# Optimization experiments

Hardware: AMD Instinct MI355X
Metric: run time of the kernel (lower is better)

## Reference

```python
import jax, jax.numpy as jnp
import numpy as np

Z_DIM, C_DIM = 256, 256
H = 96            # hidden_size = input_size = out_channel_num
L = 4             # num_layers
T = 239           # seq_len
B = 4096          # batch


def _gru_layer(x_seq, h0, wi, wh, bi, bh):
    """PyTorch-convention GRU layer. x_seq: [T,B,H], h0: [B,H].
    wi, wh: [3H,H] ordered (r,z,n); bi, bh: [3H]."""
    gi_seq = jnp.einsum('tbh,gh->tbg', x_seq, wi) + bi  # [T,B,3H], precomputed

    def step(h, gi):
        gh = h @ wh.T + bh
        i_r, i_z, i_n = jnp.split(gi, 3, axis=-1)
        h_r, h_z, h_n = jnp.split(gh, 3, axis=-1)
        r = jax.nn.sigmoid(i_r + h_r)
        z = jax.nn.sigmoid(i_z + h_z)
        n = jnp.tanh(i_n + r * h_n)
        h_new = (1.0 - z) * n + z * h
        return h_new, h_new

    _, out = jax.lax.scan(step, h0, gi_seq)
    return out  # [T,B,H]


def setup_inputs() -> dict:
    key = jax.random.key(0)
    ks = jax.random.split(key, 8)
    z = jax.random.normal(ks[0], (B, Z_DIM), dtype=jnp.float32)
    c = jax.random.normal(ks[1], (B, C_DIM), dtype=jnp.float32)
    s_fc = 1.0 / np.sqrt(Z_DIM + C_DIM)
    s_h = 1.0 / np.sqrt(H)
    fc1_w = jax.random.normal(ks[2], (L * H, Z_DIM + C_DIM), dtype=jnp.float32) * s_fc
    fc1_b = jax.random.normal(ks[3], (L * H,), dtype=jnp.float32) * s_fc
    w_ih = jax.random.normal(ks[4], (L, 3 * H, H), dtype=jnp.float32) * s_h
    w_hh = jax.random.normal(ks[5], (L, 3 * H, H), dtype=jnp.float32) * s_h
    b_ih = jax.random.normal(ks[6], (L, 3 * H), dtype=jnp.float32) * s_h
    b_hh = jax.random.normal(ks[7], (L, 3 * H), dtype=jnp.float32) * s_h
    return {"z": z, "c": c, "fc1_w": fc1_w, "fc1_b": fc1_b,
            "w_ih": w_ih, "w_hh": w_hh, "b_ih": b_ih, "b_hh": b_hh}


def reference(z, c, fc1_w, fc1_b, w_ih, w_hh, b_ih, b_hh):
    x = jnp.concatenate((z, c), axis=1)                 # [B, 512]
    h = x @ fc1_w.T + fc1_b                             # [B, 4H]
    h = jnp.where(h >= 0, h, 0.2 * h)                   # LeakyReLU(0.2)
    h0 = h.reshape(L, x.shape[0], H)                    # matches torch .view(L,B,H)
    seq = jnp.zeros((T, x.shape[0], H), dtype=x.dtype)  # GRU input is zeros
    for l in range(L):
        seq = _gru_layer(seq, h0[l], w_ih[l], w_hh[l], b_ih[l], b_hh[l])
    # fc2 output is computed but discarded in the original forward
    return jnp.transpose(seq, (1, 2, 0))                # [B, H, T]
```

## Files before the change

### kernel.cpp

```cpp
#include <hip/hip_runtime.h>
#include <stdint.h>

#define HDIM 96
#define G3   288
#define TLEN 239
#define BB   16
#define NBLK 256
#define NTHR 768

typedef _Float16 f16;
typedef f16  f16x8 __attribute__((ext_vector_type(8)));
typedef f16  f16x4 __attribute__((ext_vector_type(4)));
typedef float f32x4 __attribute__((ext_vector_type(4)));

__device__ __forceinline__ float sigm(float x)  { return 1.f / (1.f + __expf(-x)); }
__device__ __forceinline__ float tanh_(float x) { return 1.f - 2.f / (1.f + __expf(2.f * x)); }

template<bool HAS_X>
__global__ __launch_bounds__(NTHR, 3)
void gru_layer(float* seq,
               const float* __restrict__ zin, const float* __restrict__ cin,
               const float* __restrict__ fc1w, const float* __restrict__ fc1b,
               const float* __restrict__ wih, const float* __restrict__ whh,
               const float* __restrict__ bih, const float* __restrict__ bhh,
               int layer)
{
  __shared__ f16   h_plane[2][16][104];
  __shared__ float gi_buf[16][300];
  __shared__ float xcat[4][512];
  __shared__ float fc1o[4][384];

  const int tid = threadIdx.x;
  const int wv  = tid >> 6;
  const int ln  = tid & 63;
  const int r0  = blockIdx.x * BB;
  const int g   = ln >> 4;
  const int lm  = ln & 15;

  const int base_in = layer * 1024 + (r0 >> 2);
  for (int i = tid; i < 4 * 512; i += NTHR) {
    int q = i >> 9, k = i & 511;
    xcat[q][k] = (k < 256) ? zin[(base_in + q) * 256 + k]
                           : cin[(base_in + q) * 256 + (k - 256)];
  }
  __syncthreads();
  for (int of = wv * 32; of < wv * 32 + 32; ++of) {
    float wreg[8];
    #pragma unroll
    for (int i = 0; i < 8; ++i) wreg[i] = fc1w[of * 512 + ln + 64 * i];
    float s[4];
    #pragma unroll
    for (int q = 0; q < 4; ++q) {
      float a = 0.f;
      #pragma unroll
      for (int i = 0; i < 8; ++i) a += wreg[i] * xcat[q][ln + 64 * i];
      s[q] = a;
    }
    #pragma unroll
    for (int off = 32; off; off >>= 1)
      #pragma unroll
      for (int q = 0; q < 4; ++q) s[q] += __shfl_down(s[q], off);
    if (ln == 0) {
      float b = fc1b[of];
      #pragma unroll
      for (int q = 0; q < 4; ++q) {
        float v = s[q] + b;
        fc1o[q][of] = (v >= 0.f) ? v : 0.2f * v;
      }
    }
  }
  __syncthreads();

  const bool is_gh = (wv < 6);
  const int  wg    = is_gh ? wv : wv - 6;
  const int  col   = wg * 16 + lm;

  f16x8 wf[3][3];
  if (is_gh || HAS_X) {
    const float* wmat = is_gh ? whh : wih;
    #pragma unroll
    for (int nt = 0; nt < 3; ++nt)
      #pragma unroll
      for (int kt = 0; kt < 3; ++kt) {
        const float* src = wmat + (nt * 96 + col) * 96 + kt * 32 + 4 * g;
        f16x8 f;
        #pragma unroll
        for (int j = 0; j < 4; ++j) { f[j] = (f16)src[j]; f[4 + j] = (f16)src[16 + j]; }
        wf[nt][kt] = f;
      }
  }

  float bir = 0, biz = 0, bin_ = 0, bhr = 0, bhz = 0, bhn = 0;
  float hprev[4] = {0, 0, 0, 0};
  uint32_t obase[4] = {0, 0, 0, 0};
  if (is_gh) {
    bir = bih[col]; biz = bih[96 + col]; bin_ = bih[192 + col];
    bhr = bhh[col]; bhz = bhh[96 + col]; bhn = bhh[192 + col];
    #pragma unroll
    for (int j = 0; j < 4; ++j) {
      float h0v = fc1o[g][j * 96 + col];
      hprev[j] = h0v;
      h_plane[0][4 * g + j][col] = (f16)h0v;
      obase[j] = ((uint32_t)(r0 + 4 * g + j) * 96 + col) * 239;
    }
  }

  const float* xptr[6];
  float xc[6][4];
  if (!is_gh && HAS_X) {
    #pragma unroll
    for (int kt = 0; kt < 3; ++kt)
      #pragma unroll
      for (int hh = 0; hh < 2; ++hh) {
        int k = kt * 32 + 16 * hh + 4 * g;
        xptr[kt * 2 + hh] = seq + ((size_t)(r0 + lm) * 96 + k) * 239;
      }
    #pragma unroll
    for (int f = 0; f < 6; ++f)
      #pragma unroll
      for (int j = 0; j < 4; ++j) xc[f][j] = xptr[f][j * 239];
  }
  __syncthreads();

  float hist[4][8];
  for (int t0 = 0; t0 < TLEN; t0 += 8) {
    const int nsteps = (TLEN - t0 < 8) ? (TLEN - t0) : 8;
    #pragma unroll
    for (int s = 0; s < 8; ++s) {
      if (s < nsteps) {
        const int t = t0 + s;
        const int buf = t & 1;
        const f32x4 z4 = {0.f, 0.f, 0.f, 0.f};
        f32x4 acc[3] = {z4, z4, z4};

        if (is_gh) {
          #pragma unroll
          for (int kt = 0; kt < 3; ++kt) {
            f16x4 lo = *(const f16x4*)&h_plane[buf][lm][kt * 32 + 4 * g];
            f16x4 hi = *(const f16x4*)&h_plane[buf][lm][kt * 32 + 16 + 4 * g];
            f16x8 a;
            #pragma unroll
            for (int j = 0; j < 4; ++j) { a[j] = lo[j]; a[4 + j] = hi[j]; }
            #pragma unroll
            for (int nt = 0; nt < 3; ++nt)
              acc[nt] = __builtin_amdgcn_mfma_f32_16x16x32_f16(a, wf[nt][kt], acc[nt], 0, 0, 0);
          }
        } else if (HAS_X) {
          #pragma unroll
          for (int kt = 0; kt < 3; ++kt) {
            f16x8 a;
            #pragma unroll
            for (int j = 0; j < 4; ++j) { a[j] = (f16)xc[2 * kt][j]; a[4 + j] = (f16)xc[2 * kt + 1][j]; }
            #pragma unroll
            for (int nt = 0; nt < 3; ++nt)
              acc[nt] = __builtin_amdgcn_mfma_f32_16x16x32_f16(a, wf[nt][kt], acc[nt], 0, 0, 0);
          }
          #pragma unroll
          for (int nt = 0; nt < 3; ++nt)
            #pragma unroll
            for (int reg = 0; reg < 4; ++reg)
              gi_buf[4 * g + reg][nt * 96 + col] = acc[nt][reg];
          if (t + 1 < TLEN) {
            #pragma unroll
            for (int f = 0; f < 6; ++f)
              #pragma unroll
              for (int j = 0; j < 4; ++j) xc[f][j] = xptr[f][(t + 1) + j * 239];
          }
        }
        __syncthreads();

        if (is_gh) {
          #pragma unroll
          for (int reg = 0; reg < 4; ++reg) {
            float gr = acc[0][reg] + bhr;
            float gz = acc[1][reg] + bhz;
            float gn = acc[2][reg] + bhn;
            float ir = bir, iz = biz, in_ = bin_;
            if (HAS_X) {
              ir  += gi_buf[4 * g + reg][col];
              iz  += gi_buf[4 * g + reg][96 + col];
              in_ += gi_buf[4 * g + reg][192 + col];
            }
            float r  = sigm(ir + gr);
            float zg = sigm(iz + gz);
            float n  = tanh_(in_ + r * gn);
            float hn = (1.f - zg) * n + zg * hprev[reg];
            hprev[reg] = hn;
            hist[reg][s] = hn;
            h_plane[buf ^ 1][4 * g + reg][col] = (f16)hn;
          }
        }
        __syncthreads();
      }
    }
    if (is_gh) {
      #pragma unroll
      for (int reg = 0; reg < 4; ++reg)
        #pragma unroll
        for (int q = 0; q < 8; ++q)
          if (q < nsteps) seq[obase[reg] + (uint32_t)(t0 + q)] = hist[reg][q];
    }
  }
}

extern "C" void kernel_launch(void* const* d_in, const int* in_sizes, int n_in,
                              void* d_out, int out_size, void* d_ws, size_t ws_size,
                              hipStream_t stream) {
  const float* zin  = (const float*)d_in[0];
  const float* cin  = (const float*)d_in[1];
  const float* fc1w = (const float*)d_in[2];
  const float* fc1b = (const float*)d_in[3];
  const float* wih  = (const float*)d_in[4];
  const float* whh  = (const float*)d_in[5];
  const float* bih  = (const float*)d_in[6];
  const float* bhh  = (const float*)d_in[7];
  float* seq = (float*)d_out;
  (void)d_ws; (void)ws_size; (void)in_sizes; (void)n_in; (void)out_size;

  dim3 grid(NBLK), blk(NTHR);
  gru_layer<false><<<grid, blk, 0, stream>>>(seq, zin, cin, fc1w, fc1b,
                                             wih, whh, bih, bhh, 0);
  for (int l = 1; l < 4; ++l)
    gru_layer<true><<<grid, blk, 0, stream>>>(seq, zin, cin, fc1w, fc1b,
                                              wih + l * G3 * HDIM, whh + l * G3 * HDIM,
                                              bih + l * G3, bhh + l * G3, l);
}
```

Baseline: 12.55 ms.

## Store intermediate GRU layers as time-major fp16 in workspace, transpose final output via LDS

Intermediate layer outputs are now written as fp16 in a time-major [T,B,H] layout, in the workspace and in the unused second half of the output buffer. The next layer reads them as contiguous vector loads, double-buffered two steps ahead, instead of reading fp32 elements at a stride of 239. The final layer keeps a 32-step ring of hidden states in LDS and writes 32-step chunks to the [B,H,T] output with nontemporal stores. The aim is to cut uncoalesced global traffic and halve the bytes moved between layers. In exchange the final output is rounded through fp16, the LDS footprint grows a lot, and the old in-place path remains only as a fallback when the workspace is too small.

Result: slower. 19.94 ms (+58.8%).

```diff
diff --git a/kernel.cpp b/kernel.cpp
--- a/kernel.cpp
+++ b/kernel.cpp
@@ -7,6 +7,10 @@
 #define BB   16
 #define NBLK 256
 #define NTHR 768
+#define TSLAB (4096 * 96)
+
+#define HSLOT 1668
+#define HROW  104
 
 typedef _Float16 f16;
 typedef f16  f16x8 __attribute__((ext_vector_type(8)));
@@ -16,16 +20,16 @@
 __device__ __forceinline__ float sigm(float x)  { return 1.f / (1.f + __expf(-x)); }
 __device__ __forceinline__ float tanh_(float x) { return 1.f - 2.f / (1.f + __expf(2.f * x)); }
 
-template<bool HAS_X>
+template<bool HAS_X, bool FINAL_OUT>
 __global__ __launch_bounds__(NTHR, 3)
-void gru_layer(float* seq,
-               const float* __restrict__ zin, const float* __restrict__ cin,
-               const float* __restrict__ fc1w, const float* __restrict__ fc1b,
-               const float* __restrict__ wih, const float* __restrict__ whh,
-               const float* __restrict__ bih, const float* __restrict__ bhh,
-               int layer)
+void gru_layer_tm(const f16* __restrict__ xin, void* __restrict__ outp,
+                  const float* __restrict__ zin, const float* __restrict__ cin,
+                  const float* __restrict__ fc1w, const float* __restrict__ fc1b,
+                  const float* __restrict__ wih, const float* __restrict__ whh,
+                  const float* __restrict__ bih, const float* __restrict__ bhh,
+                  int layer)
 {
-  __shared__ f16   h_plane[2][16][104];
+  __shared__ f16   hbuf[32][HSLOT];
   __shared__ float gi_buf[16][300];
   __shared__ float xcat[4][512];
   __shared__ float fc1o[4][384];
@@ -92,6 +96,203 @@
 
   float bir = 0, biz = 0, bin_ = 0, bhr = 0, bhz = 0, bhn = 0;
   float hprev[4] = {0, 0, 0, 0};
+  if (is_gh) {
+    bir = bih[col]; biz = bih[96 + col]; bin_ = bih[192 + col];
+    bhr = bhh[col]; bhz = bhh[96 + col]; bhn = bhh[192 + col];
+    #pragma unroll
+    for (int j = 0; j < 4; ++j) {
+      float h0v = fc1o[g][j * 96 + col];
+      hprev[j] = h0v;
+      hbuf[31][(4 * g + j) * HROW + col] = (f16)h0v;
+    }
+  }
+
+  f16x4 xa[2][6];
+  size_t xoff = (size_t)(r0 + lm) * 96;
+  if (!is_gh && HAS_X) {
+    #pragma unroll
+    for (int pb = 0; pb < 2; ++pb) {
+      const f16* p = xin + (size_t)pb * TSLAB + xoff;
+      #pragma unroll
+      for (int kt = 0; kt < 3; ++kt) {
+        xa[pb][kt * 2]     = *(const f16x4*)(p + kt * 32 + 4 * g);
+        xa[pb][kt * 2 + 1] = *(const f16x4*)(p + kt * 32 + 16 + 4 * g);
+      }
+    }
+  }
+  __syncthreads();
+
+  f16*   out16 = (f16*)outp;
+  float* outf  = (float*)outp;
+
+  for (int t = 0; t < TLEN; ++t) {
+    const int slot_r = (t + 31) & 31;
+    const int slot_w = t & 31;
+    const f32x4 z4 = {0.f, 0.f, 0.f, 0.f};
+    f32x4 acc[3] = {z4, z4, z4};
+
+    if (is_gh) {
+      #pragma unroll
+      for (int kt = 0; kt < 3; ++kt) {
+        f16x4 lo = *(const f16x4*)&hbuf[slot_r][lm * HROW + kt * 32 + 4 * g];
+        f16x4 hi = *(const f16x4*)&hbuf[slot_r][lm * HROW + kt * 32 + 16 + 4 * g];
+        f16x8 a;
+        #pragma unroll
+        for (int j = 0; j < 4; ++j) { a[j] = lo[j]; a[4 + j] = hi[j]; }
+        #pragma unroll
+        for (int nt = 0; nt < 3; ++nt)
+          acc[nt] = __builtin_amdgcn_mfma_f32_16x16x32_f16(a, wf[nt][kt], acc[nt], 0, 0, 0);
+      }
+    } else if (HAS_X) {
+      const int cur = t & 1;
+      #pragma unroll
+      for (int kt = 0; kt < 3; ++kt) {
+        f16x4 lo = xa[cur][kt * 2], hi = xa[cur][kt * 2 + 1];
+        f16x8 a;
+        #pragma unroll
+        for (int j = 0; j < 4; ++j) { a[j] = lo[j]; a[4 + j] = hi[j]; }
+        #pragma unroll
+        for (int nt = 0; nt < 3; ++nt)
+          acc[nt] = __builtin_amdgcn_mfma_f32_16x16x32_f16(a, wf[nt][kt], acc[nt], 0, 0, 0);
+      }
+      #pragma unroll
+      for (int nt = 0; nt < 3; ++nt)
+        #pragma unroll
+        for (int reg = 0; reg < 4; ++reg)
+          gi_buf[4 * g + reg][nt * 96 + col] = acc[nt][reg];
+      if (t + 2 < TLEN) {
+        const f16* p = xin + (size_t)(t + 2) * TSLAB + xoff;
+        #pragma unroll
+        for (int kt = 0; kt < 3; ++kt) {
+          xa[cur][kt * 2]     = *(const f16x4*)(p + kt * 32 + 4 * g);
+          xa[cur][kt * 2 + 1] = *(const f16x4*)(p + kt * 32 + 16 + 4 * g);
+        }
+      }
+    }
+    __syncthreads();
+
+    if (is_gh) {
+      #pragma unroll
+      for (int reg = 0; reg < 4; ++reg) {
+        float gr = acc[0][reg] + bhr;
+        float gz = acc[1][reg] + bhz;
+        float gn = acc[2][reg] + bhn;
+        float ir = bir, iz = biz, in_ = bin_;
+        if (HAS_X) {
+          ir  += gi_buf[4 * g + reg][col];
+          iz  += gi_buf[4 * g + reg][96 + col];
+          in_ += gi_buf[4 * g + reg][192 + col];
+        }
+        float r  = sigm(ir + gr);
+        float zg = sigm(iz + gz);
+        float n  = tanh_(in_ + r * gn);
+        float hn = (1.f - zg) * n + zg * hprev[reg];
+        hprev[reg] = hn;
+        f16 h16 = (f16)hn;
+        hbuf[slot_w][(4 * g + reg) * HROW + col] = h16;
+        if (!FINAL_OUT)
+          __builtin_nontemporal_store(
+              h16, &out16[(size_t)t * TSLAB + (r0 + 4 * g + reg) * 96 + col]);
+      }
+    }
+    __syncthreads();
+
+    if (FINAL_OUT && (((t & 31) == 31) || (t == TLEN - 1))) {
+      const int t0 = t & ~31;
+      const int ns = t - t0 + 1;
+      const int tl = ln & 31;
+      const int hw = ln >> 5;
+      if (tl < ns) {
+        #pragma unroll 4
+        for (int i = 0; i < 64; ++i) {
+          int rc   = wv * 128 + i * 2 + hw;
+          int brow = (rc * 683) >> 16;
+          int c    = rc - brow * 96;
+          float v  = (float)hbuf[tl][brow * HROW + c];
+          __builtin_nontemporal_store(
+              v, &outf[((uint32_t)(r0 + brow) * 96 + c) * 239 + t0 + tl]);
+        }
+      }
+    }
+  }
+}
+
+template<bool HAS_X>
+__global__ __launch_bounds__(NTHR, 3)
+void gru_layer_ip(float* seq,
+                  const float* __restrict__ zin, const float* __restrict__ cin,
+                  const float* __restrict__ fc1w, const float* __restrict__ fc1b,
+                  const float* __restrict__ wih, const float* __restrict__ whh,
+                  const float* __restrict__ bih, const float* __restrict__ bhh,
+                  int layer)
+{
+  __shared__ f16   h_plane[2][16][104];
+  __shared__ float gi_buf[16][300];
+  __shared__ float xcat[4][512];
+  __shared__ float fc1o[4][384];
+
+  const int tid = threadIdx.x;
+  const int wv  = tid >> 6;
+  const int ln  = tid & 63;
+  const int r0  = blockIdx.x * BB;
+  const int g   = ln >> 4;
+  const int lm  = ln & 15;
+
+  const int base_in = layer * 1024 + (r0 >> 2);
+  for (int i = tid; i < 4 * 512; i += NTHR) {
+    int q = i >> 9, k = i & 511;
+    xcat[q][k] = (k < 256) ? zin[(base_in + q) * 256 + k]
+                           : cin[(base_in + q) * 256 + (k - 256)];
+  }
+  __syncthreads();
+  for (int of = wv * 32; of < wv * 32 + 32; ++of) {
+    float wreg[8];
+    #pragma unroll
+    for (int i = 0; i < 8; ++i) wreg[i] = fc1w[of * 512 + ln + 64 * i];
+    float s[4];
+    #pragma unroll
+    for (int q = 0; q < 4; ++q) {
+      float a = 0.f;
+      #pragma unroll
+      for (int i = 0; i < 8; ++i) a += wreg[i] * xcat[q][ln + 64 * i];
+      s[q] = a;
+    }
+    #pragma unroll
+    for (int off = 32; off; off >>= 1)
+      #pragma unroll
+      for (int q = 0; q < 4; ++q) s[q] += __shfl_down(s[q], off);
+    if (ln == 0) {
+      float b = fc1b[of];
+      #pragma unroll
+      for (int q = 0; q < 4; ++q) {
+        float v = s[q] + b;
+        fc1o[q][of] = (v >= 0.f) ? v : 0.2f * v;
+      }
+    }
+  }
+  __syncthreads();
+
+  const bool is_gh = (wv < 6);
+  const int  wg    = is_gh ? wv : wv - 6;
+  const int  col   = wg * 16 + lm;
+
+  f16x8 wf[3][3];
+  if (is_gh || HAS_X) {
+    const float* wmat = is_gh ? whh : wih;
+    #pragma unroll
+    for (int nt = 0; nt < 3; ++nt)
+      #pragma unroll
+      for (int kt = 0; kt < 3; ++kt) {
+        const float* src = wmat + (nt * 96 + col) * 96 + kt * 32 + 4 * g;
+        f16x8 f;
+        #pragma unroll
+        for (int j = 0; j < 4; ++j) { f[j] = (f16)src[j]; f[4 + j] = (f16)src[16 + j]; }
+        wf[nt][kt] = f;
+      }
+  }
+
+  float bir = 0, biz = 0, bin_ = 0, bhr = 0, bhz = 0, bhn = 0;
+  float hprev[4] = {0, 0, 0, 0};
   uint32_t obase[4] = {0, 0, 0, 0};
   if (is_gh) {
     bir = bih[col]; biz = bih[96 + col]; bin_ = bih[192 + col];
@@ -111,10 +312,8 @@
     #pragma unroll
     for (int kt = 0; kt < 3; ++kt)
       #pragma unroll
-      for (int hh = 0; hh < 2; ++hh) {
-        int k = kt * 32 + 16 * hh + 4 * g;
-        xptr[kt * 2 + hh] = seq + ((size_t)(r0 + lm) * 96 + k) * 239;
-      }
+      for (int hh = 0; hh < 2; ++hh)
+        xptr[kt * 2 + hh] = seq + ((size_t)(r0 + lm) * 96 + kt * 32 + 16 * hh + 4 * g) * 239;
     #pragma unroll
     for (int f = 0; f < 6; ++f)
       #pragma unroll
@@ -132,7 +331,6 @@
         const int buf = t & 1;
         const f32x4 z4 = {0.f, 0.f, 0.f, 0.f};
         f32x4 acc[3] = {z4, z4, z4};
-
         if (is_gh) {
           #pragma unroll
           for (int kt = 0; kt < 3; ++kt) {
@@ -168,7 +366,6 @@
           }
         }
         __syncthreads();
-
         if (is_gh) {
           #pragma unroll
           for (int reg = 0; reg < 4; ++reg) {
@@ -214,14 +411,32 @@
   const float* whh  = (const float*)d_in[5];
   const float* bih  = (const float*)d_in[6];
   const float* bhh  = (const float*)d_in[7];
-  float* seq = (float*)d_out;
-  (void)d_ws; (void)ws_size; (void)in_sizes; (void)n_in; (void)out_size;
-
+  (void)in_sizes; (void)n_in; (void)out_size;
+
+  const size_t need = (size_t)TLEN * TSLAB * sizeof(f16);
   dim3 grid(NBLK), blk(NTHR);
-  gru_layer<false><<<grid, blk, 0, stream>>>(seq, zin, cin, fc1w, fc1b,
-                                             wih, whh, bih, bhh, 0);
-  for (int l = 1; l < 4; ++l)
-    gru_layer<true><<<grid, blk, 0, stream>>>(seq, zin, cin, fc1w, fc1b,
-                                              wih + l * G3 * HDIM, whh + l * G3 * HDIM,
-                                              bih + l * G3, bhh + l * G3, l);
+
+  if (ws_size >= need) {
+    f16* bufA = (f16*)d_ws;
+    f16* bufB = (f16*)((char*)d_out + need);
+    gru_layer_tm<false, false><<<grid, blk, 0, stream>>>(
+        nullptr, bufA, zin, cin, fc1w, fc1b, wih, whh, bih, bhh, 0);
+    gru_layer_tm<true, false><<<grid, blk, 0, stream>>>(
+        bufA, bufB, zin, cin, fc1w, fc1b,
+        wih + 1 * G3 * HDIM, whh + 1 * G3 * HDIM, bih + 1 * G3, bhh + 1 * G3, 1);
+    gru_layer_tm<true, false><<<grid, blk, 0, stream>>>(
+        bufB, bufA, zin, cin, fc1w, fc1b,
+        wih + 2 * G3 * HDIM, whh + 2 * G3 * HDIM, bih + 2 * G3, bhh + 2 * G3, 2);
+    gru_layer_tm<true, true><<<grid, blk, 0, stream>>>(
+        bufA, d_out, zin, cin, fc1w, fc1b,
+        wih + 3 * G3 * HDIM, whh + 3 * G3 * HDIM, bih + 3 * G3, bhh + 3 * G3, 3);
+  } else {
+    float* seq = (float*)d_out;
+    gru_layer_ip<false><<<grid, blk, 0, stream>>>(seq, zin, cin, fc1w, fc1b,
+                                                  wih, whh, bih, bhh, 0);
+    for (int l = 1; l < 4; ++l)
+      gru_layer_ip<true><<<grid, blk, 0, stream>>>(seq, zin, cin, fc1w, fc1b,
+                                                   wih + l * G3 * HDIM, whh + l * G3 * HDIM,
+                                                   bih + l * G3, bhh + l * G3, l);
+  }
 }
```
